# Performance work log

Hardware: AMD Instinct MI355X
Metric: run time of the kernel (lower is better)

## Reference

```python
import jax, jax.numpy as jnp
import numpy as np

B = 4096; NINP = 512; NHID = 2048
NBI = 1; NBO = 8; TOPK = 4; NMRI = 2
BSO = NHID // NBO           # 256 (block_size_out)
ATT_OUT = BSO * 4           # 1024
GRU_NINP = ATT_OUT * NBO    # 8192
BSI = GRU_NINP // NBO       # 1024 (GRU per-block input size)
DK_I = 64                   # inp_att d_k (n_head=1)
NH_M = 4; DK_M = 16; DV_M = 16  # mha heads/dims


def setup_inputs() -> dict:
    key = jax.random.key(0)
    ks = jax.random.split(key, 16)
    r = lambda i, shape, s=0.01: (s * jax.random.normal(ks[i], shape)).astype(jnp.float32)
    return {
        "inp": jax.random.normal(ks[0], (B, NBI * NINP), dtype=jnp.float32),
        "hx": jax.random.normal(ks[1], (B, NHID), dtype=jnp.float32),
        "cx": jax.random.normal(ks[2], (B, NHID), dtype=jnp.float32),
        "step": 0,
        # inp_att (GroupLinear q over NBO blocks; k,v over NMRI write slots; fc out)
        "Wq_i": r(3, (NBO, BSO, DK_I)),
        "Wk_i": r(4, (NMRI, NINP, DK_I)),
        "Wv_i": r(5, (NMRI, NINP, ATT_OUT)),
        "fc_i_w": r(6, (ATT_OUT, ATT_OUT), 0.02),
        "fc_i_b": jnp.zeros((ATT_OUT,), jnp.float32),
        # mha (communication attention among blocks)
        "Wq_m": r(7, (NBO, BSO, NH_M * DK_M)),
        "Wk_m": r(8, (NBO, BSO, NH_M * DK_M)),
        "Wv_m": r(9, (NBO, BSO, NH_M * DV_M)),
        "fc_m_w": r(10, (NH_M * DV_M, BSO), 0.05),
        "fc_m_b": jnp.zeros((BSO,), jnp.float32),
        "gate_m_w": r(11, (NH_M * DV_M, BSO), 0.05),
        "gate_m_b": jnp.zeros((BSO,), jnp.float32),
        # block-diagonal GRU cell (blockified params: only diagonal blocks kept)
        "Wih": r(12, (NBO, 3 * BSO, BSI), 0.02),
        "Whh": r(13, (NBO, 3 * BSO, BSO), 0.02),
        "bih": jnp.zeros((NBO, 3 * BSO), jnp.float32),
        "bhh": jnp.zeros((NBO, 3 * BSO), jnp.float32),
    }


def _forward(inp, hx, cx, Wq_i, Wk_i, Wv_i, fc_i_w, fc_i_b, Wq_m, Wk_m, Wv_m,
             fc_m_w, fc_m_b, gate_m_w, gate_m_b, Wih, Whh, bih, bhh):
    b = inp.shape[0]
    # --- build read slots: slot 0 = zeros (null), slot 1 = input ---
    x = inp.reshape(b, NBI, NINP)
    x = jnp.tile(x, (1, NMRI - 1, 1))
    x = jnp.concatenate([jnp.zeros_like(x[:, :1]), x], axis=1)            # (b, NMRI, ninp)
    hx3 = hx.reshape(b, NBO, BSO)
    # --- inp_att: n_head=1, residual=False (gate_fc unused); Sparse_attention no-op (topk>=len_k) ---
    q = jnp.einsum('bni,nio->bno', hx3, Wq_i)                             # (b, NBO, DK_I)
    k = jnp.einsum('bni,nio->bno', x, Wk_i)                               # (b, NMRI, DK_I)
    v = jnp.einsum('bni,nio->bno', x, Wv_i)                               # (b, NMRI, ATT_OUT)
    iatt = jax.nn.softmax(jnp.einsum('bqd,bkd->bqk', q, k) / float(np.sqrt(DK_I)), axis=-1)
    inp_use = jnp.einsum('bqk,bkv->bqv', iatt, v)                         # (b, NBO, ATT_OUT)
    inp_use = (inp_use @ fc_i_w + fc_i_b).reshape(b, NBO * ATT_OUT)
    # --- top-k block mask: zero out the (NBO-TOPK) blocks most attentive to the null slot ---
    drop_idx = jax.lax.top_k(iatt[:, :, 0], NBO - TOPK)[1]                # (b, NBO-TOPK)
    mask = jnp.ones((b, NBO), inp.dtype).at[jnp.arange(b)[:, None], drop_idx].set(0.0)
    mask = jax.lax.stop_gradient(mask)                                    # mask.detach()
    mask_w = jnp.repeat(mask[:, :, None], BSO, axis=2).reshape(b, NHID)
    # --- block-diagonal GRUCell: h' = (1-z)*n + z*h ---
    x3 = inp_use.reshape(b, NBO, BSI)
    gx = jnp.einsum('bki,koi->bko', x3, Wih) + bih                        # (b, NBO, 3*BSO)
    gh = jnp.einsum('bkj,koj->bko', hx3, Whh) + bhh
    xr, xz, xn = jnp.split(gx, 3, axis=-1)
    hr, hz, hn = jnp.split(gh, 3, axis=-1)
    r = jax.nn.sigmoid(xr + hr)
    z = jax.nn.sigmoid(xz + hz)
    n = jnp.tanh(xn + r * hn)
    h_new = (1.0 - z) * n + z * hx3                                       # (b, NBO, BSO)
    # --- step attention among blocks; blocked_grad = identity fwd, grad*mask bwd ---
    m3 = mask[:, :, None]
    hg = m3 * h_new + jax.lax.stop_gradient((1.0 - m3) * h_new)
    qm = jnp.einsum('bni,nio->bno', hg, Wq_m).reshape(b, NBO, NH_M, DK_M)
    km = jnp.einsum('bni,nio->bno', hg, Wk_m).reshape(b, NBO, NH_M, DK_M)
    vm = jnp.einsum('bni,nio->bno', hg, Wv_m).reshape(b, NBO, NH_M, DV_M)
    am = jax.nn.softmax(jnp.einsum('bqhd,bkhd->bhqk', qm, km) / float(np.sqrt(DK_M)), axis=-1)
    om = jnp.einsum('bhqk,bkhd->bqhd', am, vm).reshape(b, NBO, NH_M * DV_M)
    att = jax.nn.sigmoid(om @ gate_m_w + gate_m_b) * jnp.tanh(om @ fc_m_w + fc_m_b)  # residual=True gating
    h_new = (h_new + att).reshape(b, NHID)
    # --- gated state update (GRU: cx_new = hx_new) ---
    hx_out = mask_w * h_new + (1.0 - mask_w) * hx
    cx_out = mask_w * h_new + (1.0 - mask_w) * cx
    return hx_out, cx_out, mask_w


def reference(inp, hx, cx, step, Wq_i, Wk_i, Wv_i, fc_i_w, fc_i_b, Wq_m, Wk_m, Wv_m,
              fc_m_w, fc_m_b, gate_m_w, gate_m_b, Wih, Whh, bih, bhh):
    del step  # unused by the math
    return _forward(inp, hx, cx, Wq_i, Wk_i, Wv_i, fc_i_w, fc_i_b, Wq_m, Wk_m, Wv_m,
                    fc_m_w, fc_m_b, gate_m_w, gate_m_b, Wih, Whh, bih, bhh)
```

## Files before the change

### kernel.cpp

```cpp
#include <hip/hip_runtime.h>
#include <hip/hip_bf16.h>

#define B_SZ 4096
#define NHID_ 2048

typedef __bf16 bf16x8 __attribute__((ext_vector_type(8)));
typedef float f32x4 __attribute__((ext_vector_type(4)));

__device__ __forceinline__ float sigmoidf_(float x) { return 1.f / (1.f + expf(-x)); }

#define GLDS16(gp, lp) __builtin_amdgcn_global_load_lds( \
    (const __attribute__((address_space(1))) void*)(gp), \
    (__attribute__((address_space(3))) void*)(lp), 16, 0, 0)

__global__ __launch_bounds__(256) void prep_all(
    const float* __restrict__ Wih, const float* __restrict__ fc_i_b,
    const float* __restrict__ bih, __hip_bfloat16* __restrict__ Wihb,
    float* __restrict__ cb,
    const float* __restrict__ inp, __hip_bfloat16* __restrict__ inpb,
    const float* __restrict__ Whh, __hip_bfloat16* __restrict__ Whhb,
    const float* __restrict__ WvBsrc, __hip_bfloat16* __restrict__ WvB,
    const float* __restrict__ fc_i_w, __hip_bfloat16* __restrict__ fcT,
    const float* __restrict__ Wq_m, const float* __restrict__ Wk_m,
    const float* __restrict__ Wv_m, __hip_bfloat16* __restrict__ WmT,
    const float* __restrict__ fc_m_w, const float* __restrict__ gate_m_w,
    __hip_bfloat16* __restrict__ fcgT)
{
    __shared__ float smem[32 * 33];
    const int bid = blockIdx.x;
    const int tid = threadIdx.x;

    if (bid < 6144) {
        long j = bid;
        const float* row = Wih + j * 1024;
        __hip_bfloat16* drow = Wihb + j * 1024;
        int i = tid * 4;
        float4 v = *(const float4*)(row + i);
        __hip_bfloat16 b0 = __float2bfloat16(v.x);
        __hip_bfloat16 b1 = __float2bfloat16(v.y);
        __hip_bfloat16 b2 = __float2bfloat16(v.z);
        __hip_bfloat16 b3 = __float2bfloat16(v.w);
        ushort4 u;
        u.x = *(unsigned short*)&b0; u.y = *(unsigned short*)&b1;
        u.z = *(unsigned short*)&b2; u.w = *(unsigned short*)&b3;
        *(ushort4*)(drow + i) = u;
        float s = fc_i_b[i] * v.x + fc_i_b[i + 1] * v.y +
                  fc_i_b[i + 2] * v.z + fc_i_b[i + 3] * v.w;
#pragma unroll
        for (int off = 32; off > 0; off >>= 1) s += __shfl_xor(s, off, 64);
        if ((tid & 63) == 0) smem[tid >> 6] = s;
        __syncthreads();
        if (tid == 0) cb[j] = smem[0] + smem[1] + smem[2] + smem[3] + bih[j];
    } else if (bid < 10240) {
        long i = (long)(bid - 6144) * 256 + tid;
        const float* src; __hip_bfloat16* dst; long off;
        if (i < 524288)       { src = inp;    dst = inpb; off = i; }
        else if (i < 917504)  { src = Whh;    dst = Whhb; off = i - 524288; }
        else                  { src = WvBsrc; dst = WvB;  off = i - 917504; }
        float4 v = ((const float4*)src)[off];
        __hip_bfloat16 b0 = __float2bfloat16(v.x);
        __hip_bfloat16 b1 = __float2bfloat16(v.y);
        __hip_bfloat16 b2 = __float2bfloat16(v.z);
        __hip_bfloat16 b3 = __float2bfloat16(v.w);
        ushort4 u;
        u.x = *(unsigned short*)&b0; u.y = *(unsigned short*)&b1;
        u.z = *(unsigned short*)&b2; u.w = *(unsigned short*)&b3;
        ((ushort4*)dst)[off] = u;
    } else if (bid < 11264) {
        int lb = bid - 10240;
        int r0 = (lb >> 5) * 32, c0 = (lb & 31) * 32;
        int tx = tid & 31, ty = tid >> 5;
        float (*tile)[33] = (float(*)[33])smem;
#pragma unroll
        for (int i = 0; i < 4; ++i)
            tile[ty + i * 8][tx] = fc_i_w[(long)(r0 + ty + i * 8) * 1024 + c0 + tx];
        __syncthreads();
#pragma unroll
        for (int i = 0; i < 4; ++i)
            fcT[(long)(c0 + ty + i * 8) * 1024 + r0 + tx] =
                __float2bfloat16(tile[tx][ty + i * 8]);
    } else if (bid < 11648) {
        int lb = bid - 11264;
        int z = lb >> 4, rem = lb & 15;
        int by = rem >> 1, bx = rem & 1;
        int which = z >> 3, nb = z & 7;
        const float* src = (which == 0) ? Wq_m : (which == 1) ? Wk_m : Wv_m;
        src += (long)nb * 16384;
        __hip_bfloat16* dst = WmT + (long)nb * 49152 + which * 64 * 256;
        int r0 = by * 32, c0 = bx * 32;
        int tx = tid & 31, ty = tid >> 5;
        float (*tile)[33] = (float(*)[33])smem;
#pragma unroll
        for (int i = 0; i < 4; ++i)
            tile[ty + i * 8][tx] = src[(long)(r0 + ty + i * 8) * 64 + c0 + tx];
        __syncthreads();
#pragma unroll
        for (int i = 0; i < 4; ++i)
            dst[(long)(c0 + ty + i * 8) * 256 + r0 + tx] =
                __float2bfloat16(tile[tx][ty + i * 8]);
    } else {
        int t = (bid - 11648) * 256 + tid;
        int np = t >> 6, k = t & 63;
        int o = (np >> 5) * 16 + (np & 15);
        const float* src = ((np >> 4) & 1) ? gate_m_w : fc_m_w;
        fcgT[t] = __float2bfloat16(src[k * 256 + o]);
    }
}

#define GM_BM 64
#define GM_BN 64
#define GM_BK 16

__global__ __launch_bounds__(256) void gemm_nn(
    const float* __restrict__ A, const float* __restrict__ Bm, float* __restrict__ C,
    int M, int N, int K, int lda, int ldb, int ldc,
    long sA, long sB, long sC)
{
    const int z = blockIdx.z;
    A += (long)z * sA; Bm += (long)z * sB; C += (long)z * sC;
    const int m0 = blockIdx.y * GM_BM;
    const int n0 = blockIdx.x * GM_BN;
    const int tid = threadIdx.x;
    const int tx = tid & 15;
    const int ty = tid >> 4;

    __shared__ float As[GM_BK][GM_BM + 4];
    __shared__ float Bs[GM_BK][GM_BN + 4];

    float acc[4][4] = {};

    for (int k0 = 0; k0 < K; k0 += GM_BK) {
#pragma unroll
        for (int i = 0; i < 4; ++i) {
            int idx = tid + i * 256;
            int r = idx >> 4, c = idx & 15;
            As[c][r] = A[(long)(m0 + r) * lda + k0 + c];
        }
#pragma unroll
        for (int i = 0; i < 4; ++i) {
            int idx = tid + i * 256;
            int r = idx >> 6, c = idx & 63;
            Bs[r][c] = Bm[(long)(k0 + r) * ldb + n0 + c];
        }
        __syncthreads();
#pragma unroll
        for (int kk = 0; kk < GM_BK; ++kk) {
            float4 a4 = *(const float4*)&As[kk][ty * 4];
            float4 b4 = *(const float4*)&Bs[kk][tx * 4];
            float av[4] = {a4.x, a4.y, a4.z, a4.w};
            float bv[4] = {b4.x, b4.y, b4.z, b4.w};
#pragma unroll
            for (int i = 0; i < 4; ++i)
#pragma unroll
                for (int j = 0; j < 4; ++j)
                    acc[i][j] += av[i] * bv[j];
        }
        __syncthreads();
    }
#pragma unroll
    for (int i = 0; i < 4; ++i) {
        long m = m0 + ty * 4 + i;
#pragma unroll
        for (int j = 0; j < 4; ++j) {
            int n = n0 + tx * 4 + j;
            C[m * ldc + n] = acc[i][j];
        }
    }
}

__global__ __launch_bounds__(256) void gemm_nt_f32(
    const float* __restrict__ A, int lda,
    const float* __restrict__ BT, int ldb,
    float* __restrict__ C, int ldc, int K, long sB, long sC)
{
    BT += (long)blockIdx.z * sB;
    C  += (long)blockIdx.z * sC;
    const int m0 = blockIdx.y * 64;
    const int n0 = blockIdx.x * 64;
    const int tid = threadIdx.x;
    const int tx = tid & 15;
    const int ty = tid >> 4;

    __shared__ float As[16][68];
    __shared__ float Bs[64][17];

    float acc[4][4] = {};

    for (int k0 = 0; k0 < K; k0 += 16) {
#pragma unroll
        for (int i = 0; i < 4; ++i) {
            int idx = tid + i * 256;
            int r = idx >> 4, c = idx & 15;
            As[c][r] = A[(long)(m0 + r) * lda + k0 + c];
        }
#pragma unroll
        for (int i = 0; i < 4; ++i) {
            int idx = tid + i * 256;
            int r = idx >> 4, c = idx & 15;
            Bs[r][c] = BT[(long)(n0 + r) * ldb + k0 + c];
        }
        __syncthreads();
#pragma unroll
        for (int kk = 0; kk < 16; ++kk) {
            float4 a4 = *(const float4*)&As[kk][ty * 4];
            float av[4] = {a4.x, a4.y, a4.z, a4.w};
            float bv[4];
#pragma unroll
            for (int j = 0; j < 4; ++j) bv[j] = Bs[tx * 4 + j][kk];
#pragma unroll
            for (int i = 0; i < 4; ++i)
#pragma unroll
                for (int j = 0; j < 4; ++j)
                    acc[i][j] += av[i] * bv[j];
        }
        __syncthreads();
    }
#pragma unroll
    for (int i = 0; i < 4; ++i) {
        long m = m0 + ty * 4 + i;
#pragma unroll
        for (int j = 0; j < 4; ++j) {
            int n = n0 + tx * 4 + j;
            C[m * ldc + n] = acc[i][j];
        }
    }
}

__global__ __launch_bounds__(256) void s1_mask_fused(
    const float* __restrict__ hx,
    const float* __restrict__ p,
    float* __restrict__ a_buf, float* __restrict__ mask_buf,
    __hip_bfloat16* __restrict__ hxb)
{
    const int wave = threadIdx.x >> 6;
    const int lane = threadIdx.x & 63;
    const long b = (long)blockIdx.x * 4 + wave;
    const long base = b * 2048 + lane * 4;
    float s1v[8];
#pragma unroll
    for (int n = 0; n < 8; ++n) {
        float4 hv = *(const float4*)(hx + base + n * 256);
        float4 pv = *(const float4*)(p + base + n * 256);
        __hip_bfloat16 c0 = __float2bfloat16(hv.x);
        __hip_bfloat16 c1 = __float2bfloat16(hv.y);
        __hip_bfloat16 c2 = __float2bfloat16(hv.z);
        __hip_bfloat16 c3 = __float2bfloat16(hv.w);
        ushort4 u;
        u.x = *(unsigned short*)&c0; u.y = *(unsigned short*)&c1;
        u.z = *(unsigned short*)&c2; u.w = *(unsigned short*)&c3;
        *(ushort4*)(hxb + base + n * 256) = u;
        float s = hv.x * pv.x + hv.y * pv.y + hv.z * pv.z + hv.w * pv.w;
#pragma unroll
        for (int off = 32; off > 0; off >>= 1) s += __shfl_xor(s, off, 64);
        s1v[n] = s * 0.125f;
    }
    unsigned maskbits = 0;
#pragma unroll
    for (int n = 0; n < 8; ++n) {
        int rank = 0;
#pragma unroll
        for (int m = 0; m < 8; ++m) {
            if (m == n) continue;
            if (s1v[m] < s1v[n] || (s1v[m] == s1v[n] && m < n)) rank++;
        }
        if (rank >= 4) maskbits |= (1u << n);
    }
    if (lane < 8) {
        float sv = s1v[0];
#pragma unroll
        for (int n = 1; n < 8; ++n)
            if (lane == n) sv = s1v[n];
        a_buf[b * 8 + lane] = sigmoidf_(sv);
        mask_buf[b * 8 + lane] = ((maskbits >> lane) & 1u) ? 1.0f : 0.0f;
    }
}

__global__ __launch_bounds__(256) void gemm_mfma_obf16(
    const __hip_bfloat16* __restrict__ A, int lda,
    const __hip_bfloat16* __restrict__ BT, int ldb,
    __hip_bfloat16* __restrict__ C, int ldc, int K,
    long sA, long sB, long sC)
{
    A  += (long)blockIdx.z * sA;
    BT += (long)blockIdx.z * sB;
    C  += (long)blockIdx.z * sC;
    const int m0 = blockIdx.y * 128;
    const int n0 = blockIdx.x * 64;
    const int tid = threadIdx.x;
    const int lane = tid & 63, wid = tid >> 6;
    const int wr = wid >> 1, wc = wid & 1;
    const int l15 = lane & 15, l4 = lane >> 4;

    __shared__ __align__(16) char lds_raw[16384 + 8192];
    char* Alds = lds_raw;
    char* Blds = lds_raw + 16384;

    f32x4 acc[4][2] = {};

    for (int k0 = 0; k0 < K; k0 += 64) {
#pragma unroll
        for (int ii = 0; ii < 4; ++ii) {
            int issue = ii * 4 + wid;
            int chunk = issue * 64 + lane;
            int r = chunk >> 3, cs = chunk & 7;
            int cl = cs ^ (r & 7);
            const __hip_bfloat16* g = A + (long)(m0 + r) * lda + k0 + cl * 8;
            GLDS16(g, Alds + issue * 1024);
        }
#pragma unroll
        for (int jj = 0; jj < 2; ++jj) {
            int issue = jj * 4 + wid;
            int chunk = issue * 64 + lane;
            int r = chunk >> 3, cs = chunk & 7;
            int cl = cs ^ (r & 7);
            const __hip_bfloat16* g = BT + (long)(n0 + r) * ldb + k0 + cl * 8;
            GLDS16(g, Blds + issue * 1024);
        }
        __syncthreads();
#pragma unroll
        for (int kk = 0; kk < 2; ++kk) {
            bf16x8 af[4], bfr[2];
#pragma unroll
            for (int im = 0; im < 4; ++im) {
                int r = wr * 64 + im * 16 + l15;
                int cl = (kk * 4 + l4) ^ (l15 & 7);
                af[im] = *(const bf16x8*)(Alds + r * 128 + cl * 16);
            }
#pragma unroll
            for (int jn = 0; jn < 2; ++jn) {
                int r = wc * 32 + jn * 16 + l15;
                int cl = (kk * 4 + l4) ^ (l15 & 7);
                bfr[jn] = *(const bf16x8*)(Blds + r * 128 + cl * 16);
            }
#pragma unroll
            for (int im = 0; im < 4; ++im)
#pragma unroll
                for (int jn = 0; jn < 2; ++jn)
                    acc[im][jn] = __builtin_amdgcn_mfma_f32_16x16x32_bf16(
                        af[im], bfr[jn], acc[im][jn], 0, 0, 0);
        }
        __syncthreads();
    }
#pragma unroll
    for (int im = 0; im < 4; ++im)
#pragma unroll
        for (int reg = 0; reg < 4; ++reg) {
            long m = m0 + wr * 64 + im * 16 + l4 * 4 + reg;
#pragma unroll
            for (int jn = 0; jn < 2; ++jn) {
                int n = n0 + wc * 32 + jn * 16 + l15;
                C[m * ldc + n] = __float2bfloat16(acc[im][jn][reg]);
            }
        }
}

__global__ __launch_bounds__(256) void gemm_mfma_qkv(
    const __hip_bfloat16* __restrict__ hnewb,
    const __hip_bfloat16* __restrict__ WmT,
    __hip_bfloat16* __restrict__ qout)
{
    const int z = blockIdx.z;
    const int m0 = blockIdx.y * 128;
    const int n0 = blockIdx.x * 64;
    const int tid = threadIdx.x;
    const int lane = tid & 63, wid = tid >> 6;
    const int wr = wid >> 1, wc = wid & 1;
    const int l15 = lane & 15, l4 = lane >> 4;

    const __hip_bfloat16* A = hnewb + z * 256;
    const __hip_bfloat16* BT = WmT + (long)z * 192 * 256;

    __shared__ __align__(16) char lds_raw[16384 + 8192];
    char* Alds = lds_raw;
    char* Blds = lds_raw + 16384;

    f32x4 acc[4][2] = {};

    for (int k0 = 0; k0 < 256; k0 += 64) {
#pragma unroll
        for (int ii = 0; ii < 4; ++ii) {
            int issue = ii * 4 + wid;
            int chunk = issue * 64 + lane;
            int r = chunk >> 3, cs = chunk & 7;
            int cl = cs ^ (r & 7);
            const __hip_bfloat16* g = A + (long)(m0 + r) * 2048 + k0 + cl * 8;
            GLDS16(g, Alds + issue * 1024);
        }
#pragma unroll
        for (int jj = 0; jj < 2; ++jj) {
            int issue = jj * 4 + wid;
            int chunk = issue * 64 + lane;
            int r = chunk >> 3, cs = chunk & 7;
            int cl = cs ^ (r & 7);
            const __hip_bfloat16* g = BT + (long)(n0 + r) * 256 + k0 + cl * 8;
            GLDS16(g, Blds + issue * 1024);
        }
        __syncthreads();
#pragma unroll
        for (int kk = 0; kk < 2; ++kk) {
            bf16x8 af[4], bfr[2];
#pragma unroll
            for (int im = 0; im < 4; ++im) {
                int r = wr * 64 + im * 16 + l15;
                int cl = (kk * 4 + l4) ^ (l15 & 7);
                af[im] = *(const bf16x8*)(Alds + r * 128 + cl * 16);
            }
#pragma unroll
            for (int jn = 0; jn < 2; ++jn) {
                int r = wc * 32 + jn * 16 + l15;
                int cl = (kk * 4 + l4) ^ (l15 & 7);
                bfr[jn] = *(const bf16x8*)(Blds + r * 128 + cl * 16);
            }
#pragma unroll
            for (int im = 0; im < 4; ++im)
#pragma unroll
                for (int jn = 0; jn < 2; ++jn)
                    acc[im][jn] = __builtin_amdgcn_mfma_f32_16x16x32_bf16(
                        af[im], bfr[jn], acc[im][jn], 0, 0, 0);
        }
        __syncthreads();
    }
#pragma unroll
    for (int jn = 0; jn < 2; ++jn) {
        int j = n0 + wc * 32 + jn * 16 + l15;
        int g = j >> 6, d = j & 63;
        __hip_bfloat16* outp = qout + (long)g * 2097152 + (long)z * 64 + d;
#pragma unroll
        for (int im = 0; im < 4; ++im)
#pragma unroll
            for (int reg = 0; reg < 4; ++reg) {
                long m = m0 + wr * 64 + im * 16 + l4 * 4 + reg;
                outp[m * 512] = __float2bfloat16(acc[im][jn][reg]);
            }
    }
}

__global__ __launch_bounds__(512) void gru_fused_mfma(
    const __hip_bfloat16* __restrict__ inpb,
    const __hip_bfloat16* __restrict__ hxb,
    const float* __restrict__ a_buf,
    const float* __restrict__ cb,
    const __hip_bfloat16* __restrict__ W2T,
    const __hip_bfloat16* __restrict__ Whhb,
    const float* __restrict__ bhh,
    __hip_bfloat16* __restrict__ hnewb)
{
    const int bid = blockIdx.x;
    const int kblk = bid & 7;
    const int r_ = bid >> 3;
    const int ol0 = (r_ & 7) * 32;
    const int m0 = (r_ >> 3) * 128;
    const int tid = threadIdx.x;
    const int lane = tid & 63, wid = tid >> 6;
    const int wr = wid >> 1;
    const int wc = wid & 1;
    const int l15 = lane & 15, l4 = lane >> 4;

    __shared__ __align__(16) char lds_raw[2 * 28672];

    f32x4 accx[2][3] = {};
    f32x4 acch[2][3] = {};

    const __hip_bfloat16* W2 = W2T + (long)kblk * 768 * 512;
    const __hip_bfloat16* Wh = Whhb + (long)kblk * 768 * 256;
    const __hip_bfloat16* hxk = hxb + kblk * 256;

    const int iiA0 = wid, iiA1 = wid + 8;
    const int cA0 = iiA0 * 64 + lane, rA0 = cA0 >> 3, clA0 = (cA0 & 7) ^ (rA0 & 7);
    const int cA1 = iiA1 * 64 + lane, rA1 = cA1 >> 3, clA1 = (cA1 & 7) ^ (rA1 & 7);
    const int jjB0 = wid, jjB1 = wid + 8;
    const int cB0 = jjB0 * 64 + lane, rB0 = cB0 >> 3, clB0 = (cB0 & 7) ^ (rB0 & 7);
    const int cB1 = jjB1 * 64 + lane, rB1 = cB1 >> 3, clB1 = (cB1 & 7) ^ (rB1 & 7);
    const bool hasB1 = (wid < 4);
    const int gg0 = rB0 >> 5, oll0 = rB0 & 31;
    const int gg1 = (rB1 >> 5) & 3, oll1 = rB1 & 31;
    const int dA0 = iiA0 * 1024, dA1 = iiA1 * 1024;
    const int dB0 = 16384 + jjB0 * 1024, dB1 = 16384 + jjB1 * 1024;

    const __hip_bfloat16* pA0 = inpb + (long)(m0 + rA0) * 512 + clA0 * 8;
    const __hip_bfloat16* pA1 = inpb + (long)(m0 + rA1) * 512 + clA1 * 8;
    const __hip_bfloat16* pB0 = W2 + (long)(gg0 * 256 + ol0 + oll0) * 512 + clB0 * 8;
    const __hip_bfloat16* pB1 = W2 + (long)(gg1 * 256 + ol0 + oll1) * 512 + clB1 * 8;

#define STAGE4(buf) do {                                                       \
    char* L = lds_raw + (buf) * 28672;                                         \
    GLDS16(pA0, L + dA0);                                                      \
    GLDS16(pA1, L + dA1);                                                      \
    GLDS16(pB0, L + dB0);                                                      \
    if (hasB1) GLDS16(pB1, L + dB1);                                           \
    pA0 += 64; pA1 += 64; pB0 += 64; pB1 += 64;                                \
} while (0)

    int offA[2][2], offB[2][3];
#pragma unroll
    for (int kk = 0; kk < 2; ++kk) {
        int cl = (kk * 4 + l4) ^ (l15 & 7);
#pragma unroll
        for (int im = 0; im < 2; ++im)
            offA[kk][im] = (wr * 32 + im * 16 + l15) * 128 + cl * 16;
#pragma unroll
        for (int g = 0; g < 3; ++g)
            offB[kk][g] = 16384 + (g * 32 + wc * 16 + l15) * 128 + cl * 16;
    }

#define COMPUTE(acc, buf) do {                                                 \
    char* L = lds_raw + (buf) * 28672;                                         \
    _Pragma("unroll") for (int kk = 0; kk < 2; ++kk) {                         \
        bf16x8 af[2], bfr[3];                                                  \
        _Pragma("unroll") for (int im = 0; im < 2; ++im)                       \
            af[im] = *(const bf16x8*)(L + offA[kk][im]);                       \
        _Pragma("unroll") for (int g = 0; g < 3; ++g)                          \
            bfr[g] = *(const bf16x8*)(L + offB[kk][g]);                        \
        _Pragma("unroll") for (int im = 0; im < 2; ++im)                       \
            _Pragma("unroll") for (int g = 0; g < 3; ++g)                      \
                acc[im][g] = __builtin_amdgcn_mfma_f32_16x16x32_bf16(          \
                    af[im], bfr[g], acc[im][g], 0, 0, 0);                      \
    }                                                                          \
} while (0)

    STAGE4(0);
    asm volatile("s_waitcnt vmcnt(0)" ::: "memory");
    __syncthreads();

    int cur = 0;
    for (int t = 0; t < 8; ++t) {
        if (t < 7) {
            STAGE4(cur ^ 1);
        } else {
            pA0 = hxk + (long)(m0 + rA0) * 2048 + clA0 * 8;
            pA1 = hxk + (long)(m0 + rA1) * 2048 + clA1 * 8;
            pB0 = Wh + (long)(gg0 * 256 + ol0 + oll0) * 256 + clB0 * 8;
            pB1 = Wh + (long)(gg1 * 256 + ol0 + oll1) * 256 + clB1 * 8;
            STAGE4(cur ^ 1);
        }
        __builtin_amdgcn_s_setprio(1);
        COMPUTE(accx, cur);
        __builtin_amdgcn_s_setprio(0);
        asm volatile("s_waitcnt vmcnt(0)" ::: "memory");
        __syncthreads();
        cur ^= 1;
    }
    for (int t = 0; t < 4; ++t) {
        if (t < 3) STAGE4(cur ^ 1);
        __builtin_amdgcn_s_setprio(1);
        COMPUTE(acch, cur);
        __builtin_amdgcn_s_setprio(0);
        asm volatile("s_waitcnt vmcnt(0)" ::: "memory");
        __syncthreads();
        cur ^= 1;
    }
#undef STAGE4
#undef COMPUTE

    const int ol = ol0 + wc * 16 + l15;
    const float* cbk = cb + kblk * 768;
    const float cb0 = cbk[ol], cb1 = cbk[256 + ol], cb2 = cbk[512 + ol];
    const float* bhk = bhh + kblk * 768;
    const float bh0 = bhk[ol], bh1 = bhk[256 + ol], bh2 = bhk[512 + ol];
#pragma unroll
    for (int im = 0; im < 2; ++im) {
#pragma unroll
        for (int reg = 0; reg < 4; ++reg) {
            long m = m0 + wr * 32 + im * 16 + l4 * 4 + reg;
            float av = a_buf[m * 8 + kblk];
            float gx0 = av * accx[im][0][reg] + cb0;
            float gx1 = av * accx[im][1][reg] + cb1;
            float gx2 = av * accx[im][2][reg] + cb2;
            float gh0 = acch[im][0][reg] + bh0;
            float gh1 = acch[im][1][reg] + bh1;
            float gh2 = acch[im][2][reg] + bh2;
            float rr = sigmoidf_(gx0 + gh0);
            float zz = sigmoidf_(gx1 + gh1);
            float nn = tanhf(gx2 + rr * gh2);
            long idx = m * 2048 + kblk * 256 + ol;
            float hxv = __bfloat162float(hxb[idx]);
            hnewb[idx] = __float2bfloat16((1.f - zz) * nn + zz * hxv);
        }
    }
}

__global__ __launch_bounds__(256) void mattn_kernel(
    const __hip_bfloat16* __restrict__ qm, const __hip_bfloat16* __restrict__ km,
    const __hip_bfloat16* __restrict__ vm, __hip_bfloat16* __restrict__ omb)
{
    const int t = threadIdx.x;
    const int local = t & 31;
    const long b = (long)blockIdx.x * 8 + (t >> 5);
    const int h = local >> 3, qn = local & 7;
    const long base = b * 512 + h * 16;

    float qv[16];
#pragma unroll
    for (int i = 0; i < 2; ++i) {
        bf16x8 v = *(const bf16x8*)(qm + base + qn * 64 + i * 8);
#pragma unroll
        for (int j = 0; j < 8; ++j) qv[i * 8 + j] = (float)v[j];
    }
    float sc[8];
#pragma unroll
    for (int kn = 0; kn < 8; ++kn) {
        float s = 0.f;
#pragma unroll
        for (int i = 0; i < 2; ++i) {
            bf16x8 v = *(const bf16x8*)(km + base + kn * 64 + i * 8);
#pragma unroll
            for (int j = 0; j < 8; ++j) s += qv[i * 8 + j] * (float)v[j];
        }
        sc[kn] = s * 0.25f;
    }
    float mx = sc[0];
#pragma unroll
    for (int kn = 1; kn < 8; ++kn) mx = fmaxf(mx, sc[kn]);
    float ssum = 0.f;
#pragma unroll
    for (int kn = 0; kn < 8; ++kn) { sc[kn] = expf(sc[kn] - mx); ssum += sc[kn]; }
    float inv = 1.f / ssum;

    float acc[16] = {};
#pragma unroll
    for (int kn = 0; kn < 8; ++kn) {
        float w = sc[kn] * inv;
#pragma unroll
        for (int i = 0; i < 2; ++i) {
            bf16x8 v = *(const bf16x8*)(vm + base + kn * 64 + i * 8);
#pragma unroll
            for (int j = 0; j < 8; ++j) acc[i * 8 + j] += w * (float)v[j];
        }
    }
#pragma unroll
    for (int i = 0; i < 2; ++i) {
        bf16x8 o;
#pragma unroll
        for (int j = 0; j < 8; ++j) o[j] = (__bf16)acc[i * 8 + j];
        *(bf16x8*)(omb + base + qn * 64 + i * 8) = o;
    }
}

__global__ __launch_bounds__(256) void att_final(
    const __hip_bfloat16* __restrict__ omb,
    const __hip_bfloat16* __restrict__ fcgT,
    const float* __restrict__ fc_b, const float* __restrict__ gate_b,
    const __hip_bfloat16* __restrict__ hnewb,
    const float* __restrict__ maskb,
    const float* __restrict__ hx, const float* __restrict__ cx,
    float* __restrict__ hx_out, float* __restrict__ cx_out,
    float* __restrict__ mask_w)
{
    const int m0 = blockIdx.y * 128;
    const int n0 = blockIdx.x * 64;
    const int tid = threadIdx.x;
    const int lane = tid & 63, wid = tid >> 6;
    const int wr = wid >> 1, wc = wid & 1;
    const int l15 = lane & 15, l4 = lane >> 4;

    __shared__ __align__(16) char lds_raw[16384 + 8192];
    char* Alds = lds_raw;
    char* Blds = lds_raw + 16384;

    f32x4 acc[4][2] = {};
#pragma unroll
    for (int ii = 0; ii < 4; ++ii) {
        int issue = ii * 4 + wid;
        int chunk = issue * 64 + lane;
        int r = chunk >> 3, cs = chunk & 7;
        int cl = cs ^ (r & 7);
        const __hip_bfloat16* g = omb + (long)(m0 + r) * 64 + cl * 8;
        GLDS16(g, Alds + issue * 1024);
    }
#pragma unroll
    for (int jj = 0; jj < 2; ++jj) {
        int issue = jj * 4 + wid;
        int chunk = issue * 64 + lane;
        int r = chunk >> 3, cs = chunk & 7;
        int cl = cs ^ (r & 7);
        const __hip_bfloat16* g = fcgT + (long)(n0 + r) * 64 + cl * 8;
        GLDS16(g, Blds + issue * 1024);
    }
    __syncthreads();
#pragma unroll
    for (int kk = 0; kk < 2; ++kk) {
        bf16x8 af[4], bfr[2];
#pragma unroll
        for (int im = 0; im < 4; ++im) {
            int r = wr * 64 + im * 16 + l15;
            int cl = (kk * 4 + l4) ^ (l15 & 7);
            af[im] = *(const bf16x8*)(Alds + r * 128 + cl * 16);
        }
#pragma unroll
        for (int jn = 0; jn < 2; ++jn) {
            int r = wc * 32 + jn * 16 + l15;
            int cl = (kk * 4 + l4) ^ (l15 & 7);
            bfr[jn] = *(const bf16x8*)(Blds + r * 128 + cl * 16);
        }
#pragma unroll
        for (int im = 0; im < 4; ++im)
#pragma unroll
            for (int jn = 0; jn < 2; ++jn)
                acc[im][jn] = __builtin_amdgcn_mfma_f32_16x16x32_bf16(
                    af[im], bfr[jn], acc[im][jn], 0, 0, 0);
    }
    const int o = ((n0 + wc * 32) >> 1) + l15;
    const float fb = fc_b[o], gb = gate_b[o];
#pragma unroll
    for (int im = 0; im < 4; ++im)
#pragma unroll
        for (int reg = 0; reg < 4; ++reg) {
            long m = m0 + wr * 64 + im * 16 + l4 * 4 + reg;
            long idx = m * 256 + o;
            float mv = maskb[m];
            float att = sigmoidf_(acc[im][1][reg] + gb) * tanhf(acc[im][0][reg] + fb);
            float ho, co;
            if (mv != 0.f) {
                float h2 = __bfloat162float(hnewb[idx]) + att;
                ho = h2; co = h2;
            } else {
                ho = hx[idx]; co = cx[idx];
            }
            hx_out[idx] = ho;
            cx_out[idx] = co;
            mask_w[idx] = mv;
        }
}

extern "C" void kernel_launch(void* const* d_in, const int* in_sizes, int n_in,
                              void* d_out, int out_size, void* d_ws, size_t ws_size,
                              hipStream_t stream)
{
    const float* inp     = (const float*)d_in[0];
    const float* hx      = (const float*)d_in[1];
    const float* cx      = (const float*)d_in[2];
    const float* Wq_i    = (const float*)d_in[4];
    const float* Wk_i    = (const float*)d_in[5];
    const float* Wv_i    = (const float*)d_in[6];
    const float* fc_i_w  = (const float*)d_in[7];
    const float* fc_i_b  = (const float*)d_in[8];
    const float* Wq_m    = (const float*)d_in[9];
    const float* Wk_m    = (const float*)d_in[10];
    const float* Wv_m    = (const float*)d_in[11];
    const float* fc_m_w  = (const float*)d_in[12];
    const float* fc_m_b  = (const float*)d_in[13];
    const float* gate_m_w= (const float*)d_in[14];
    const float* gate_m_b= (const float*)d_in[15];
    const float* Wih     = (const float*)d_in[16];
    const float* Whh     = (const float*)d_in[17];
    const float* bih     = (const float*)d_in[18];
    const float* bhh     = (const float*)d_in[19];

    float* out = (float*)d_out;
    const long BH = (long)B_SZ * NHID_;
    float* hx_out = out;
    float* cx_out = out + BH;
    float* mask_w = out + 2 * BH;
    __hip_bfloat16* hxb = (__hip_bfloat16*)out;
    __hip_bfloat16* qkvb = (__hip_bfloat16*)out;
    float* pbuf = cx_out;

    float* w = (float*)d_ws;
    float* a_buf = w;
    float* maskb = w + 32768;
    float* cbuf  = w + 65536;
    __hip_bfloat16* fcgT = (__hip_bfloat16*)(w + 73728);
    __hip_bfloat16* WmT  = (__hip_bfloat16*)(w + 90112);
    __hip_bfloat16* Wihb = (__hip_bfloat16*)(w + 286720);
    __hip_bfloat16* fcT  = (__hip_bfloat16*)(w + 3432448);
    __hip_bfloat16* WvB  = (__hip_bfloat16*)(w + 3956736);
    float* krow = w + 4218880;
    __hip_bfloat16* hnewb= (__hip_bfloat16*)(w + 286720);
    __hip_bfloat16* WvFTt= (__hip_bfloat16*)(w + 4481024);
    __hip_bfloat16* inpb = (__hip_bfloat16*)(w + 4743168);
    __hip_bfloat16* W2T  = (__hip_bfloat16*)(w + 5791744);
    __hip_bfloat16* Whhb = (__hip_bfloat16*)(w + 7364608);
    __hip_bfloat16* omb  = (__hip_bfloat16*)(w + 5791744);

    prep_all<<<dim3(11776), dim3(256), 0, stream>>>(
        Wih, fc_i_b, bih, Wihb, cbuf,
        inp, inpb, Whh, Whhb, Wv_i + 512 * 1024, WvB,
        fc_i_w, fcT, Wq_m, Wk_m, Wv_m, WmT, fc_m_w, gate_m_w, fcgT);
    gemm_nn<<<dim3(1, 64, 1), dim3(256), 0, stream>>>(
        inp, Wk_i + 512 * 64, krow, 4096, 64, 512, 512, 64, 64, 0, 0, 0);
    gemm_nt_f32<<<dim3(4, 64, 8), dim3(256), 0, stream>>>(
        krow, 64, Wq_i, 64, pbuf, 2048, 64, 16384, 256);
    s1_mask_fused<<<dim3(1024), dim3(256), 0, stream>>>(hx, pbuf, a_buf, maskb, hxb);
    gemm_mfma_obf16<<<dim3(16, 4, 1), dim3(256), 0, stream>>>(
        WvB, 1024, fcT, 1024, WvFTt, 1024, 1024, 0, 0, 0);
    gemm_mfma_obf16<<<dim3(8, 6, 8), dim3(256), 0, stream>>>(
        Wihb, 1024, WvFTt, 1024, W2T, 512, 1024,
        768L * 1024, 0, 768L * 512);
    gru_fused_mfma<<<dim3(2048), dim3(512), 0, stream>>>(
        inpb, hxb, a_buf, cbuf, W2T, Whhb, bhh, hnewb);
    gemm_mfma_qkv<<<dim3(3, 32, 8), dim3(256), 0, stream>>>(hnewb, WmT, qkvb);
    mattn_kernel<<<dim3(512), dim3(256), 0, stream>>>(
        qkvb, qkvb + 2097152, qkvb + 4194304, omb);
    att_final<<<dim3(8, 256, 1), dim3(256), 0, stream>>>(
        omb, fcgT, fc_m_b, gate_m_b, hnewb, maskb, hx, cx, hx_out, cx_out, mask_w);
}
```

Before: 231.6 us.

## Compute attention scores via per-block query projection; widen QKV GEMM tile to full N

The input-attention scores were computed by expanding krow·Wq_i^T into a B×2048 fp32 buffer and dotting it with hx. Now hx is projected with Wq_i into a B×8×64 query buffer and dotted with the 64-wide key row inside s1_mask_fused. This cuts the intermediate write/read traffic from 2048 to 512 floats per row. Separately, the QKV MFMA GEMM now covers all 192 output columns per block (6 N-fragments per wave) instead of splitting across 3 blocks, so the A tile is loaded once. The cost is more registers and LDS per block and fewer blocks in flight.

```diff
diff --git a/kernel.cpp b/kernel.cpp
--- a/kernel.cpp
+++ b/kernel.cpp
@@ -168,67 +168,10 @@
     }
 }
 
-__global__ __launch_bounds__(256) void gemm_nt_f32(
-    const float* __restrict__ A, int lda,
-    const float* __restrict__ BT, int ldb,
-    float* __restrict__ C, int ldc, int K, long sB, long sC)
-{
-    BT += (long)blockIdx.z * sB;
-    C  += (long)blockIdx.z * sC;
-    const int m0 = blockIdx.y * 64;
-    const int n0 = blockIdx.x * 64;
-    const int tid = threadIdx.x;
-    const int tx = tid & 15;
-    const int ty = tid >> 4;
-
-    __shared__ float As[16][68];
-    __shared__ float Bs[64][17];
-
-    float acc[4][4] = {};
-
-    for (int k0 = 0; k0 < K; k0 += 16) {
-#pragma unroll
-        for (int i = 0; i < 4; ++i) {
-            int idx = tid + i * 256;
-            int r = idx >> 4, c = idx & 15;
-            As[c][r] = A[(long)(m0 + r) * lda + k0 + c];
-        }
-#pragma unroll
-        for (int i = 0; i < 4; ++i) {
-            int idx = tid + i * 256;
-            int r = idx >> 4, c = idx & 15;
-            Bs[r][c] = BT[(long)(n0 + r) * ldb + k0 + c];
-        }
-        __syncthreads();
-#pragma unroll
-        for (int kk = 0; kk < 16; ++kk) {
-            float4 a4 = *(const float4*)&As[kk][ty * 4];
-            float av[4] = {a4.x, a4.y, a4.z, a4.w};
-            float bv[4];
-#pragma unroll
-            for (int j = 0; j < 4; ++j) bv[j] = Bs[tx * 4 + j][kk];
-#pragma unroll
-            for (int i = 0; i < 4; ++i)
-#pragma unroll
-                for (int j = 0; j < 4; ++j)
-                    acc[i][j] += av[i] * bv[j];
-        }
-        __syncthreads();
-    }
-#pragma unroll
-    for (int i = 0; i < 4; ++i) {
-        long m = m0 + ty * 4 + i;
-#pragma unroll
-        for (int j = 0; j < 4; ++j) {
-            int n = n0 + tx * 4 + j;
-            C[m * ldc + n] = acc[i][j];
-        }
-    }
-}
-
 __global__ __launch_bounds__(256) void s1_mask_fused(
     const float* __restrict__ hx,
-    const float* __restrict__ p,
+    const float* __restrict__ q,
+    const float* __restrict__ krow,
     float* __restrict__ a_buf, float* __restrict__ mask_buf,
     __hip_bfloat16* __restrict__ hxb)
 {
@@ -236,11 +179,11 @@
     const int lane = threadIdx.x & 63;
     const long b = (long)blockIdx.x * 4 + wave;
     const long base = b * 2048 + lane * 4;
+    const float kr = krow[b * 64 + lane];
     float s1v[8];
 #pragma unroll
     for (int n = 0; n < 8; ++n) {
         float4 hv = *(const float4*)(hx + base + n * 256);
-        float4 pv = *(const float4*)(p + base + n * 256);
         __hip_bfloat16 c0 = __float2bfloat16(hv.x);
         __hip_bfloat16 c1 = __float2bfloat16(hv.y);
         __hip_bfloat16 c2 = __float2bfloat16(hv.z);
@@ -249,10 +192,10 @@
         u.x = *(unsigned short*)&c0; u.y = *(unsigned short*)&c1;
         u.z = *(unsigned short*)&c2; u.w = *(unsigned short*)&c3;
         *(ushort4*)(hxb + base + n * 256) = u;
-        float s = hv.x * pv.x + hv.y * pv.y + hv.z * pv.z + hv.w * pv.w;
-#pragma unroll
-        for (int off = 32; off > 0; off >>= 1) s += __shfl_xor(s, off, 64);
-        s1v[n] = s * 0.125f;
+        float p = q[b * 512 + n * 64 + lane] * kr;
+#pragma unroll
+        for (int off = 32; off > 0; off >>= 1) p += __shfl_xor(p, off, 64);
+        s1v[n] = p * 0.125f;
     }
     unsigned maskbits = 0;
 #pragma unroll
@@ -361,7 +304,6 @@
 {
     const int z = blockIdx.z;
     const int m0 = blockIdx.y * 128;
-    const int n0 = blockIdx.x * 64;
     const int tid = threadIdx.x;
     const int lane = tid & 63, wid = tid >> 6;
     const int wr = wid >> 1, wc = wid & 1;
@@ -370,59 +312,54 @@
     const __hip_bfloat16* A = hnewb + z * 256;
     const __hip_bfloat16* BT = WmT + (long)z * 192 * 256;
 
-    __shared__ __align__(16) char lds_raw[16384 + 8192];
+    __shared__ __align__(16) char lds_raw[16384 + 24576];
     char* Alds = lds_raw;
     char* Blds = lds_raw + 16384;
 
-    f32x4 acc[4][2] = {};
+    f32x4 acc[4][6] = {};
 
     for (int k0 = 0; k0 < 256; k0 += 64) {
-#pragma unroll
-        for (int ii = 0; ii < 4; ++ii) {
-            int issue = ii * 4 + wid;
-            int chunk = issue * 64 + lane;
+        for (int ii = wid; ii < 16; ii += 4) {
+            int chunk = ii * 64 + lane;
             int r = chunk >> 3, cs = chunk & 7;
             int cl = cs ^ (r & 7);
             const __hip_bfloat16* g = A + (long)(m0 + r) * 2048 + k0 + cl * 8;
-            GLDS16(g, Alds + issue * 1024);
-        }
-#pragma unroll
-        for (int jj = 0; jj < 2; ++jj) {
-            int issue = jj * 4 + wid;
-            int chunk = issue * 64 + lane;
+            GLDS16(g, Alds + ii * 1024);
+        }
+        for (int jj = wid; jj < 24; jj += 4) {
+            int chunk = jj * 64 + lane;
             int r = chunk >> 3, cs = chunk & 7;
             int cl = cs ^ (r & 7);
-            const __hip_bfloat16* g = BT + (long)(n0 + r) * 256 + k0 + cl * 8;
-            GLDS16(g, Blds + issue * 1024);
+            const __hip_bfloat16* g = BT + (long)r * 256 + k0 + cl * 8;
+            GLDS16(g, Blds + jj * 1024);
         }
         __syncthreads();
 #pragma unroll
         for (int kk = 0; kk < 2; ++kk) {
-            bf16x8 af[4], bfr[2];
+            int cl = (kk * 4 + l4) ^ (l15 & 7);
+            bf16x8 af[4], bfr[6];
 #pragma unroll
             for (int im = 0; im < 4; ++im) {
                 int r = wr * 64 + im * 16 + l15;
-                int cl = (kk * 4 + l4) ^ (l15 & 7);
                 af[im] = *(const bf16x8*)(Alds + r * 128 + cl * 16);
             }
 #pragma unroll
-            for (int jn = 0; jn < 2; ++jn) {
-                int r = wc * 32 + jn * 16 + l15;
-                int cl = (kk * 4 + l4) ^ (l15 & 7);
+            for (int jn = 0; jn < 6; ++jn) {
+                int r = wc * 96 + jn * 16 + l15;
                 bfr[jn] = *(const bf16x8*)(Blds + r * 128 + cl * 16);
             }
 #pragma unroll
             for (int im = 0; im < 4; ++im)
 #pragma unroll
-                for (int jn = 0; jn < 2; ++jn)
+                for (int jn = 0; jn < 6; ++jn)
                     acc[im][jn] = __builtin_amdgcn_mfma_f32_16x16x32_bf16(
                         af[im], bfr[jn], acc[im][jn], 0, 0, 0);
         }
         __syncthreads();
     }
 #pragma unroll
-    for (int jn = 0; jn < 2; ++jn) {
-        int j = n0 + wc * 32 + jn * 16 + l15;
+    for (int jn = 0; jn < 6; ++jn) {
+        int j = wc * 96 + jn * 16 + l15;
         int g = j >> 6, d = j & 63;
         __hip_bfloat16* outp = qout + (long)g * 2097152 + (long)z * 64 + d;
 #pragma unroll
@@ -753,7 +690,7 @@
     float* mask_w = out + 2 * BH;
     __hip_bfloat16* hxb = (__hip_bfloat16*)out;
     __hip_bfloat16* qkvb = (__hip_bfloat16*)out;
-    float* pbuf = cx_out;
+    float* qbuf = cx_out;
 
     float* w = (float*)d_ws;
     float* a_buf = w;
@@ -778,9 +715,10 @@
         fc_i_w, fcT, Wq_m, Wk_m, Wv_m, WmT, fc_m_w, gate_m_w, fcgT);
     gemm_nn<<<dim3(1, 64, 1), dim3(256), 0, stream>>>(
         inp, Wk_i + 512 * 64, krow, 4096, 64, 512, 512, 64, 64, 0, 0, 0);
-    gemm_nt_f32<<<dim3(4, 64, 8), dim3(256), 0, stream>>>(
-        krow, 64, Wq_i, 64, pbuf, 2048, 64, 16384, 256);
-    s1_mask_fused<<<dim3(1024), dim3(256), 0, stream>>>(hx, pbuf, a_buf, maskb, hxb);
+    gemm_nn<<<dim3(1, 64, 8), dim3(256), 0, stream>>>(
+        hx, Wq_i, qbuf, 4096, 64, 256, 2048, 64, 512, 256, 16384, 64);
+    s1_mask_fused<<<dim3(1024), dim3(256), 0, stream>>>(
+        hx, qbuf, krow, a_buf, maskb, hxb);
     gemm_mfma_obf16<<<dim3(16, 4, 1), dim3(256), 0, stream>>>(
         WvB, 1024, fcT, 1024, WvFTt, 1024, 1024, 0, 0, 0);
     gemm_mfma_obf16<<<dim3(8, 6, 8), dim3(256), 0, stream>>>(
@@ -788,7 +726,7 @@
         768L * 1024, 0, 768L * 512);
     gru_fused_mfma<<<dim3(2048), dim3(512), 0, stream>>>(
         inpb, hxb, a_buf, cbuf, W2T, Whhb, bhh, hnewb);
-    gemm_mfma_qkv<<<dim3(3, 32, 8), dim3(256), 0, stream>>>(hnewb, WmT, qkvb);
+    gemm_mfma_qkv<<<dim3(1, 32, 8), dim3(256), 0, stream>>>(hnewb, WmT, qkvb);
     mattn_kernel<<<dim3(512), dim3(256), 0, stream>>>(
         qkvb, qkvb + 2097152, qkvb + 4194304, omb);
     att_final<<<dim3(8, 256, 1), dim3(256), 0, stream>>>(
```

After: 229.2 us. Within noise of the previous version (-1.1%).
